# Kernel optimization log

Measured on AMD Instinct MI355X. Metric: run time of the kernel, lower is better.

## Reference

```python
import jax, jax.numpy as jnp
import numpy as np
import math

B, N, KN, CIN, COUT, NC, DIM = 4, 8192, 16, 64, 64, 16, 3


def _linear_params(key, fan_in, fan_out):
    kw, kb = jax.random.split(key)
    bound = 1.0 / math.sqrt(fan_in)
    w = jax.random.uniform(kw, (fan_in, fan_out), jnp.float32, -bound, bound)
    b = jax.random.uniform(kb, (fan_out,), jnp.float32, -bound, bound)
    return w, b


def setup_inputs() -> dict:
    key = jax.random.key(0)
    ks = jax.random.split(key, 9)
    inp = jax.random.normal(ks[0], (B, N, CIN), jnp.float32)
    points = jax.random.uniform(ks[1], (B, N, DIM), jnp.float32)
    next_pts = jax.random.uniform(ks[2], (B, N, DIM), jnp.float32)
    indices = jax.random.randint(ks[3], (B, N, KN), 0, N, jnp.int64)
    wbound = math.sqrt(3.0) * math.sqrt(2.0 / (CIN + COUT))
    weight = jax.random.uniform(ks[4], (CIN, NC, COUT), jnp.float32, -wbound, wbound)
    bias = jnp.zeros((COUT,), jnp.float32)
    # centers: points inside the unit ball (scaled uniform cube is a faithful stand-in for a learned param init)
    centers = jax.random.uniform(ks[5], (DIM, NC), jnp.float32, -1.0, 1.0) / math.sqrt(DIM)
    l1_w, l1_b = _linear_params(ks[6], DIM * NC, 2 * NC)
    l2_w, l2_b = _linear_params(ks[7], 2 * NC, NC)
    l3_w, l3_b = _linear_params(ks[8], NC, NC)
    return {
        "inp": inp, "points": points, "next_pts": next_pts, "indices": indices,
        "weight": weight, "bias": bias, "centers": centers,
        "l1_w": l1_w, "l1_b": l1_b, "l2_w": l2_w, "l2_b": l2_b,
        "l3_w": l3_w, "l3_b": l3_b, "K": KN,
    }


def reference(inp, points, next_pts, indices, weight, bias, centers,
              l1_w, l1_b, l2_w, l2_b, l3_w, l3_b, K):
    b, n, cin = inp.shape
    bidx = jnp.arange(b)[:, None, None]
    feats = inp[bidx, indices]                                # [B, N, K, Cin] gather
    pts = points[bidx, indices] - next_pts[:, :, None, :]     # [B, N, K, D] relative coords
    # distances to kernel centers -> flatten to [B, N, K, D*NC]
    d = (pts[..., :, None] - centers).reshape(b, n, K, -1)
    d = jax.nn.relu(d @ l1_w + l1_b)
    d = jax.nn.relu(d @ l2_w + l2_b)
    d = jax.nn.relu(d @ l3_w + l3_b)                          # [B, N, K, NC]
    f = jnp.einsum('bnkc,bnkm->bncm', feats, d).reshape(b, n, -1)  # [B, N, Cin*NC]
    out = (f @ weight.reshape(-1, weight.shape[-1])) / K + bias    # [B, N, Cout]
    return out
```

## Files before the change

kernel.cpp:

```cpp
#include <hip/hip_runtime.h>

#define BB    4
#define NN    8192
#define KK    16
#define CIN   64
#define COUTC 64
#define P     16

typedef short bf16x8 __attribute__((ext_vector_type(8)));
typedef float f32x4  __attribute__((ext_vector_type(4)));
typedef float f32x2  __attribute__((ext_vector_type(2)));

__device__ __forceinline__ unsigned short f2bf_rne(float f) {
    unsigned int u = __builtin_bit_cast(unsigned int, f);
    u += 0x7fffu + ((u >> 16) & 1u);
    return (unsigned short)(u >> 16);
}

__device__ __forceinline__ unsigned int pack_bf2(float lo, float hi) {
    return (unsigned int)f2bf_rne(lo) | ((unsigned int)f2bf_rne(hi) << 16);
}

__global__ __launch_bounds__(256) void prep_all(
    const float* __restrict__ inp, unsigned short* __restrict__ inp_bf,
    const float* __restrict__ W, unsigned short* __restrict__ Wt,
    const float* __restrict__ l1w, const float* __restrict__ l1b,
    const float* __restrict__ centers, float* __restrict__ A1)
{
    const int blk = blockIdx.x;
    const int t   = threadIdx.x;
    if (blk < 8192) {
        const int i = blk * 256 + t;
        inp_bf[i] = f2bf_rne(inp[i]);
    } else if (blk < 8448) {
        const int o    = (blk - 8192) * 256 + t;
        const int cout = o >> 10;
        const int kp   = o & 1023;
        const int m    = kp >> 6;
        const int cin  = kp & 63;
        Wt[o] = f2bf_rne(W[(cin * 16 + m) * 64 + cout] * (1.0f / 16.0f));
    } else if (t < 32) {
        float bb = l1b[t];
        float a0 = 0.f, a1 = 0.f, a2 = 0.f;
        for (int c = 0; c < 16; ++c) {
            const float w0 = l1w[(c     ) * 32 + t];
            const float w1 = l1w[(16 + c) * 32 + t];
            const float w2 = l1w[(32 + c) * 32 + t];
            a0 += w0; a1 += w1; a2 += w2;
            bb -= centers[c] * w0 + centers[16 + c] * w1 + centers[32 + c] * w2;
        }
        A1[0 * 32 + t] = a0; A1[1 * 32 + t] = a1; A1[2 * 32 + t] = a2; A1[3 * 32 + t] = bb;
    }
}

__global__ __launch_bounds__(256, 2) void ptconv_fused(
    const unsigned short* __restrict__ inp_bf,
    const float* __restrict__ points,
    const float* __restrict__ next_pts,
    const int*   __restrict__ indices,
    const unsigned short* __restrict__ Wt,
    const float* __restrict__ A1f,
    const float* __restrict__ bias,
    const float* __restrict__ l2w, const float* __restrict__ l2b,
    const float* __restrict__ l3w, const float* __restrict__ l3b,
    float* __restrict__ out)
{
    const int t    = threadIdx.x;
    const int lane = t & 63;
    const int w    = t >> 6;
    const int pt0  = blockIdx.x * P;
    const int b    = pt0 >> 13;

    __shared__ unsigned short s_h3t[P][16][16];
    __shared__ unsigned short s_fb[P][512];

    const f32x2 zero2 = {0.f, 0.f};

    {
        const int p = t >> 4, k = t & 15;
        const int pt = pt0 + p;
        const int id = indices[(size_t)pt0 * KK + t];
        const float* pp = points + ((size_t)(b * NN + id)) * 3;
        const float* np = next_pts + (size_t)pt * 3;
        const float px = pp[0] - np[0];
        const float py = pp[1] - np[1];
        const float pz = pp[2] - np[2];
        const f32x2 px2 = {px, px}, py2 = {py, py}, pz2 = {pz, pz};

        const f32x2* A0  = (const f32x2*)(A1f);
        const f32x2* A1v = (const f32x2*)(A1f + 32);
        const f32x2* A2  = (const f32x2*)(A1f + 64);
        const f32x2* A3  = (const f32x2*)(A1f + 96);
        f32x2 h1[16];
        #pragma unroll
        for (int j = 0; j < 16; ++j) {
            f32x2 a = __builtin_elementwise_fma(pz2, A2[j], A3[j]);
            a = __builtin_elementwise_fma(py2, A1v[j], a);
            a = __builtin_elementwise_fma(px2, A0[j], a);
            h1[j] = __builtin_elementwise_max(a, zero2);
        }

        f32x2 h2[8];
        {
            const f32x2* b2p = (const f32x2*)l2b;
            #pragma unroll
            for (int j = 0; j < 8; ++j) h2[j] = b2p[j];
        }
        #pragma unroll
        for (int i = 0; i < 32; ++i) {
            const float hv = h1[i >> 1][i & 1];
            const f32x2 hvv = {hv, hv};
            const f32x2* wr = (const f32x2*)(l2w + i * 16);
            #pragma unroll
            for (int j = 0; j < 8; ++j)
                h2[j] = __builtin_elementwise_fma(hvv, wr[j], h2[j]);
        }
        #pragma unroll
        for (int j = 0; j < 8; ++j) h2[j] = __builtin_elementwise_max(h2[j], zero2);

        f32x2 h3v[8];
        {
            const f32x2* b3p = (const f32x2*)l3b;
            #pragma unroll
            for (int j = 0; j < 8; ++j) h3v[j] = b3p[j];
        }
        #pragma unroll
        for (int i = 0; i < 16; ++i) {
            const float hv = h2[i >> 1][i & 1];
            const f32x2 hvv = {hv, hv};
            const f32x2* wr = (const f32x2*)(l3w + i * 16);
            #pragma unroll
            for (int j = 0; j < 8; ++j)
                h3v[j] = __builtin_elementwise_fma(hvv, wr[j], h3v[j]);
        }
        #pragma unroll
        for (int j = 0; j < 8; ++j) {
            const f32x2 v = __builtin_elementwise_max(h3v[j], zero2);
            s_h3t[p][2 * j    ][k] = f2bf_rne(v[0]);
            s_h3t[p][2 * j + 1][k] = f2bf_rne(v[1]);
        }
    }
    __syncthreads();

    uint2 holdA[2][2], holdB[2][2];
    {
        const int arow = lane & 15;
        const int hi   = lane >> 4;
        const int kg   = (hi & 1) * 8;
        const unsigned short* ibase = inp_bf + (size_t)b * NN * 64;
        const int* idxg = indices + (size_t)pt0 * KK;
        const bf16x8 vzero = {0, 0, 0, 0, 0, 0, 0, 0};
        char* fbb = (char*)s_fb;

        #pragma unroll
        for (int pr = 0; pr < 2; ++pr) {
            const int pA  = w * 4 + pr * 2;
            const int pB  = pA + 1;
            const int myp = (hi < 2) ? pA : pB;

            int ids[8];
            #pragma unroll
            for (int jj = 0; jj < 8; ++jj) ids[jj] = idxg[myp * 16 + kg + jj];
            const unsigned short* rb[8];
            #pragma unroll
            for (int jj = 0; jj < 8; ++jj) rb[jj] = ibase + (size_t)ids[jj] * 64 + arow;

            const bf16x8 vfull = *(const bf16x8*)&s_h3t[myp][arow][kg];
            const bf16x8 bfA = (hi < 2) ? vfull : vzero;
            const bf16x8 bfB = (hi < 2) ? vzero : vfull;

            #pragma unroll
            for (int tile = 0; tile < 4; ++tile) {
                bf16x8 af;
                #pragma unroll
                for (int jj = 0; jj < 8; ++jj) af[jj] = (short)rb[jj][tile * 16];
                const f32x4 z4 = {0.f, 0.f, 0.f, 0.f};
                const f32x4 dA = __builtin_amdgcn_mfma_f32_16x16x32_bf16(af, bfA, z4, 0, 0, 0);
                const f32x4 dB = __builtin_amdgcn_mfma_f32_16x16x32_bf16(af, bfB, z4, 0, 0, 0);
                const uint2 vA = make_uint2(pack_bf2(dA[0], dA[1]), pack_bf2(dA[2], dA[3]));
                const uint2 vB = make_uint2(pack_bf2(dB[0], dB[1]), pack_bf2(dB[2], dB[3]));
                if (tile < 2) {
                    const unsigned int baseo = (unsigned)(arow * 64 + tile * 32 + hi * 8);
                    const unsigned int offA = ((unsigned)(pA * 1024) + baseo)
                                              ^ (((unsigned)((pA & 7) ^ (arow & 7))) << 4);
                    const unsigned int offB = ((unsigned)(pB * 1024) + baseo)
                                              ^ (((unsigned)((pB & 7) ^ (arow & 7))) << 4);
                    *(uint2*)(fbb + offA) = vA;
                    *(uint2*)(fbb + offB) = vB;
                } else {
                    holdA[pr][tile - 2] = vA;
                    holdB[pr][tile - 2] = vB;
                }
            }
        }
    }
    __syncthreads();

    {
        const int arow = lane & 15;
        const int hi   = lane >> 4;
        const unsigned short* wb = Wt + (size_t)(w * 16 + arow) * 1024 + hi * 8;
        const char* fbb = (const char*)s_fb;
        f32x4 acc = {0.f, 0.f, 0.f, 0.f};

        #pragma unroll
        for (int m = 0; m < 16; ++m) {
            const unsigned int xr = ((unsigned)((arow & 7) ^ (m & 7))) << 4;
            const bf16x8 av = *(const bf16x8*)(fbb +
                (((unsigned)(arow * 1024 + m * 64 + hi * 16)) ^ xr));
            const bf16x8 bv = *(const bf16x8*)(wb + m * 64);
            acc = __builtin_amdgcn_mfma_f32_16x16x32_bf16(av, bv, acc, 0, 0, 0);
        }
        __syncthreads();

        {
            char* fbw = (char*)s_fb;
            #pragma unroll
            for (int pr = 0; pr < 2; ++pr) {
                const int pA = w * 4 + pr * 2;
                const int pB = pA + 1;
                #pragma unroll
                for (int t2 = 0; t2 < 2; ++t2) {
                    const unsigned int baseo = (unsigned)(arow * 64 + t2 * 32 + hi * 8);
                    const unsigned int offA = ((unsigned)(pA * 1024) + baseo)
                                              ^ (((unsigned)((pA & 7) ^ (arow & 7))) << 4);
                    const unsigned int offB = ((unsigned)(pB * 1024) + baseo)
                                              ^ (((unsigned)((pB & 7) ^ (arow & 7))) << 4);
                    *(uint2*)(fbw + offA) = holdA[pr][t2];
                    *(uint2*)(fbw + offB) = holdB[pr][t2];
                }
            }
        }
        __syncthreads();

        #pragma unroll
        for (int m = 0; m < 16; ++m) {
            const unsigned int xr = ((unsigned)((arow & 7) ^ (m & 7))) << 4;
            const bf16x8 av = *(const bf16x8*)(fbb +
                (((unsigned)(arow * 1024 + m * 64 + hi * 16)) ^ xr));
            const bf16x8 bv = *(const bf16x8*)(wb + m * 64 + 32);
            acc = __builtin_amdgcn_mfma_f32_16x16x32_bf16(av, bv, acc, 0, 0, 0);
        }

        const float bvs = bias[w * 16 + arow];
        #pragma unroll
        for (int r = 0; r < 4; ++r) {
            const int prow = hi * 4 + r;
            out[((size_t)(pt0 + prow)) * 64 + w * 16 + arow] = acc[r] + bvs;
        }
    }
}

extern "C" void kernel_launch(void* const* d_in, const int* in_sizes, int n_in,
                              void* d_out, int out_size, void* d_ws, size_t ws_size,
                              hipStream_t stream) {
    const float* inp      = (const float*)d_in[0];
    const float* points   = (const float*)d_in[1];
    const float* next_pts = (const float*)d_in[2];
    const int*   indices  = (const int*)  d_in[3];
    const float* weight   = (const float*)d_in[4];
    const float* bias     = (const float*)d_in[5];
    const float* centers  = (const float*)d_in[6];
    const float* l1w      = (const float*)d_in[7];
    const float* l1b      = (const float*)d_in[8];
    const float* l2w      = (const float*)d_in[9];
    const float* l2b      = (const float*)d_in[10];
    const float* l3w      = (const float*)d_in[11];
    const float* l3b      = (const float*)d_in[12];
    float* outp = (float*)d_out;

    unsigned short* Wt    = (unsigned short*)d_ws;
    float*          A1f   = (float*)((char*)d_ws + 131072);
    unsigned short* inpbf = (unsigned short*)((char*)d_ws + (1 << 20));

    prep_all<<<8449, 256, 0, stream>>>(inp, inpbf, weight, Wt,
                                       l1w, l1b, centers, A1f);

    const int grid = (BB * NN) / P;
    ptconv_fused<<<grid, 256, 0, stream>>>(inpbf, points, next_pts, indices,
                                           Wt, A1f, bias,
                                           l2w, l2b, l3w, l3b, outp);
}
```

Measured before the change: 56.62 us.

## Interleave bf16 input rows for vector gathers and drop block barrier

The prep kernel now writes the bf16 copy of the input in a permuted channel order, so each lane fetches its four channel tiles with one 8-byte load per neighbour instead of four 2-byte loads. Neighbour indices are read as int4 vectors, and the s_h3t shared buffer is padded per point to reduce bank conflicts. The __syncthreads after filling s_h3t becomes a __threadfence_block. That is only safe because each wave reads back just the points it wrote itself. The aim is to cut the number of gather memory instructions and the barrier stall, at the cost of relying on that wave-local ownership.

```diff
diff --git a/kernel.cpp b/kernel.cpp
--- a/kernel.cpp
+++ b/kernel.cpp
@@ -10,6 +10,7 @@
 typedef short bf16x8 __attribute__((ext_vector_type(8)));
 typedef float f32x4  __attribute__((ext_vector_type(4)));
 typedef float f32x2  __attribute__((ext_vector_type(2)));
+typedef unsigned short u16x4 __attribute__((ext_vector_type(4)));
 
 __device__ __forceinline__ unsigned short f2bf_rne(float f) {
     unsigned int u = __builtin_bit_cast(unsigned int, f);
@@ -30,8 +31,12 @@
     const int blk = blockIdx.x;
     const int t   = threadIdx.x;
     if (blk < 8192) {
-        const int i = blk * 256 + t;
-        inp_bf[i] = f2bf_rne(inp[i]);
+        const int o  = blk * 256 + t;
+        const int n  = o >> 6;
+        const int q  = o & 63;
+        const int r  = q >> 2;
+        const int t4 = q & 3;
+        inp_bf[o] = f2bf_rne(inp[n * 64 + t4 * 16 + r]);
     } else if (blk < 8448) {
         const int o    = (blk - 8192) * 256 + t;
         const int cout = o >> 10;
@@ -71,7 +76,7 @@
     const int pt0  = blockIdx.x * P;
     const int b    = pt0 >> 13;
 
-    __shared__ unsigned short s_h3t[P][16][16];
+    __shared__ unsigned short s_h3t[P][272];
     __shared__ unsigned short s_fb[P][512];
 
     const f32x2 zero2 = {0.f, 0.f};
@@ -136,11 +141,11 @@
         #pragma unroll
         for (int j = 0; j < 8; ++j) {
             const f32x2 v = __builtin_elementwise_max(h3v[j], zero2);
-            s_h3t[p][2 * j    ][k] = f2bf_rne(v[0]);
-            s_h3t[p][2 * j + 1][k] = f2bf_rne(v[1]);
-        }
-    }
-    __syncthreads();
+            s_h3t[p][(2 * j    ) * 16 + k] = f2bf_rne(v[0]);
+            s_h3t[p][(2 * j + 1) * 16 + k] = f2bf_rne(v[1]);
+        }
+    }
+    __threadfence_block();
 
     uint2 holdA[2][2], holdB[2][2];
     {
@@ -158,14 +163,16 @@
             const int pB  = pA + 1;
             const int myp = (hi < 2) ? pA : pB;
 
-            int ids[8];
-            #pragma unroll
-            for (int jj = 0; jj < 8; ++jj) ids[jj] = idxg[myp * 16 + kg + jj];
-            const unsigned short* rb[8];
-            #pragma unroll
-            for (int jj = 0; jj < 8; ++jj) rb[jj] = ibase + (size_t)ids[jj] * 64 + arow;
-
-            const bf16x8 vfull = *(const bf16x8*)&s_h3t[myp][arow][kg];
+            const int4 i0 = *(const int4*)&idxg[myp * 16 + kg];
+            const int4 i1 = *(const int4*)&idxg[myp * 16 + kg + 4];
+            const int ids[8] = {i0.x, i0.y, i0.z, i0.w, i1.x, i1.y, i1.z, i1.w};
+
+            u16x4 rows[8];
+            #pragma unroll
+            for (int jj = 0; jj < 8; ++jj)
+                rows[jj] = *(const u16x4*)(ibase + (size_t)ids[jj] * 64 + arow * 4);
+
+            const bf16x8 vfull = *(const bf16x8*)&s_h3t[myp][arow * 16 + kg];
             const bf16x8 bfA = (hi < 2) ? vfull : vzero;
             const bf16x8 bfB = (hi < 2) ? vzero : vfull;
 
@@ -173,7 +180,7 @@
             for (int tile = 0; tile < 4; ++tile) {
                 bf16x8 af;
                 #pragma unroll
-                for (int jj = 0; jj < 8; ++jj) af[jj] = (short)rb[jj][tile * 16];
+                for (int jj = 0; jj < 8; ++jj) af[jj] = (short)rows[jj][tile];
                 const f32x4 z4 = {0.f, 0.f, 0.f, 0.f};
                 const f32x4 dA = __builtin_amdgcn_mfma_f32_16x16x32_bf16(af, bfA, z4, 0, 0, 0);
                 const f32x4 dB = __builtin_amdgcn_mfma_f32_16x16x32_bf16(af, bfB, z4, 0, 0, 0);
```

Result: no change. 56.77 us (+0.3%).
